# Optimization experiments

Measured on AMD Instinct MI355X. Metric: run time of the kernel, lower is better.

## Reference

```python
import jax, jax.numpy as jnp
import numpy as np

L, B, T, E, NH, HD, HID, V = 8, 2, 2048, 1024, 16, 64, 2816, 32000


def _rmsnorm(x, w, eps=1e-6):
    return w * (x * jax.lax.rsqrt(jnp.mean(x * x, axis=-1, keepdims=True) + eps))


def _rope(x, cos, sin):
    # x: [B,H,T,D]; cos/sin: [1,1,T,D/2]
    x1, x2 = jnp.split(x, 2, axis=-1)
    return jnp.concatenate([x1 * cos - x2 * sin, x1 * sin + x2 * cos], axis=-1)


def setup_inputs() -> dict:
    key = jax.random.key(0)
    ks = jax.random.split(key, 7)
    s = 0.02
    return {
        "idx": jax.random.randint(ks[0], (B, T), 0, V),
        "tok_emb": jax.random.normal(ks[1], (V, E), dtype=jnp.float32) * s,
        "qkv_w": jax.random.normal(ks[2], (L, 3 * E, E), dtype=jnp.float32) * s,
        "proj_w": jax.random.normal(ks[3], (L, E, E), dtype=jnp.float32) * s,
        "w1": jax.random.normal(ks[4], (L, HID, E), dtype=jnp.float32) * s,
        "w2": jax.random.normal(ks[5], (L, HID, E), dtype=jnp.float32) * s,
        "w3": jax.random.normal(ks[6], (L, E, HID), dtype=jnp.float32) * s,
        "norm1_w": jnp.ones((L, E), dtype=jnp.float32),
        "norm2_w": jnp.ones((L, E), dtype=jnp.float32),
        "norm_f_w": jnp.ones((E,), dtype=jnp.float32),
    }


def reference(idx, tok_emb, qkv_w, proj_w, w1, w2, w3, norm1_w, norm2_w, norm_f_w):
    x = tok_emb[idx]  # [B,T,E]
    # RoPE cache (start_pos=0, no kv cache -> prefill path)
    half = HD // 2
    inv_freq = 1.0 / (10000.0 ** (jnp.arange(half, dtype=jnp.float32) / half))
    pos = jnp.arange(T, dtype=jnp.float32)
    freqs = pos[:, None] * inv_freq[None, :]  # [T, D/2]
    cos = jnp.cos(freqs)[None, None]
    sin = jnp.sin(freqs)[None, None]
    causal = jnp.tril(jnp.ones((T, T), dtype=bool))
    scale = 1.0 / np.sqrt(HD).astype(np.float32)

    for l in range(L):
        # attention block
        h = _rmsnorm(x, norm1_w[l])
        qkv = h @ qkv_w[l].T  # [B,T,3E]
        q, k, v = jnp.split(qkv, 3, axis=-1)
        q = q.reshape(B, T, NH, HD).transpose(0, 2, 1, 3)
        k = k.reshape(B, T, NH, HD).transpose(0, 2, 1, 3)
        v = v.reshape(B, T, NH, HD).transpose(0, 2, 1, 3)
        q = _rope(q, cos, sin)
        k = _rope(k, cos, sin)
        att = jnp.einsum('bhqd,bhkd->bhqk', q, k) * scale
        att = jnp.where(causal, att, -jnp.inf)
        att = jax.nn.softmax(att, axis=-1)
        o = jnp.einsum('bhqk,bhkd->bhqd', att, v)
        o = o.transpose(0, 2, 1, 3).reshape(B, T, E)
        x = x + o @ proj_w[l].T
        # SwiGLU MLP
        h = _rmsnorm(x, norm2_w[l])
        x = x + (jax.nn.silu(h @ w1[l].T) * (h @ w2[l].T)) @ w3[l].T

    x = _rmsnorm(x, norm_f_w)
    logits = x @ tok_emb.T  # tied lm_head
    return logits
```

## Files before the change

### kernel.cpp

```cpp
#include <hip/hip_runtime.h>

#define GLOBAL_AS __attribute__((address_space(1)))
#define LDS_AS __attribute__((address_space(3)))

typedef unsigned short u16;
typedef unsigned int u32;
typedef __attribute__((ext_vector_type(4))) float f32x4;
typedef __attribute__((ext_vector_type(8))) short bf16x8;

#define TT 2048
#define EE 1024
#define NHH 16
#define HDD 64
#define HIDD 2816
#define VV 32000
#define MM 4096

__device__ __forceinline__ u16 f2bf(float f) {
  u32 u = __builtin_bit_cast(u32, f);
  u += 0x7fffu + ((u >> 16) & 1u);
  return (u16)(u >> 16);
}
__device__ __forceinline__ float bf2f(u16 v) {
  return __builtin_bit_cast(float, (u32)v << 16);
}


__global__ __launch_bounds__(256) void castbf_k(const float* __restrict__ in,
                                                u16* __restrict__ o, long n4) {
  const long i = (long)blockIdx.x * 256 + threadIdx.x;
  if (i >= n4) return;
  const float4 v = ((const float4*)in)[i];
  ((uint2*)o)[i] = make_uint2((u32)f2bf(v.x) | ((u32)f2bf(v.y) << 16),
                              (u32)f2bf(v.z) | ((u32)f2bf(v.w) << 16));
}

__global__ void ropetab_k(float* __restrict__ cosT, float* __restrict__ sinT) {
  const int t = blockIdx.x, j = threadIdx.x;
  const float inv = powf(10000.0f, -(float)j * (1.0f / 32.0f));
  const float f = (float)t * inv;
  cosT[t * 32 + j] = cosf(f);
  sinT[t * 32 + j] = sinf(f);
}

__global__ __launch_bounds__(256) void embed_k(const int* __restrict__ idx,
                                               const float* __restrict__ temb,
                                               float* __restrict__ x) {
  const int row = blockIdx.x;
  const int id = idx[row];
  ((float4*)(x + (size_t)row * EE))[threadIdx.x] =
      ((const float4*)(temb + (size_t)id * EE))[threadIdx.x];
}

__global__ __launch_bounds__(256) void rmsnorm_k(const float* __restrict__ x,
                                                 const float* __restrict__ w,
                                                 u16* __restrict__ o) {
  __shared__ float red[4];
  const int row = blockIdx.x, tid = threadIdx.x;
  const float4 v = ((const float4*)(x + (size_t)row * EE))[tid];
  float ss = v.x * v.x + v.y * v.y + v.z * v.z + v.w * v.w;
#pragma unroll
  for (int off = 32; off; off >>= 1) ss += __shfl_xor(ss, off, 64);
  if ((tid & 63) == 0) red[tid >> 6] = ss;
  __syncthreads();
  const float inv = rsqrtf((red[0] + red[1] + red[2] + red[3]) * (1.0f / 1024.0f) + 1e-6f);
  const float4 wv = ((const float4*)w)[tid];
  const u32 lo = (u32)f2bf(v.x * inv * wv.x) | ((u32)f2bf(v.y * inv * wv.y) << 16);
  const u32 hi = (u32)f2bf(v.z * inv * wv.z) | ((u32)f2bf(v.w * inv * wv.w) << 16);
  ((uint2*)(o + (size_t)row * EE))[tid] = make_uint2(lo, hi);
}

template <int OUTBF>
__global__ __launch_bounds__(512, 2) void gemm256p(const u16* __restrict__ A,
                                                   const u16* __restrict__ Bw,
                                                   float* __restrict__ C,
                                                   u16* __restrict__ C16,
                                                   const u16* __restrict__ G,
                                                   int N, int K) {
  __shared__ u16 lds[2 * 32768];
  const int t = threadIdx.x;
  const int lane = t & 63;
  const int wid = t >> 6;
  const int wr = wid >> 2;
  const int wc = wid & 3;
  const int l15 = lane & 15, lg = lane >> 4;
  const int bid = blockIdx.x;
  const int row0 = (bid & 15) << 8;
  const int col0 = (bid >> 4) << 8;
  const int NT = K >> 6;

  const int sr = t >> 3;
  const int su8 = (((t & 7) ^ (sr & 7)) << 3);
  const int t8 = t << 3;
  const u16* aG[4];
#pragma unroll
  for (int ga = 0; ga < 4; ++ga)
    aG[ga] = A + (size_t)(row0 + ga * 64 + sr) * K + su8;
  const u16* bG[4];
#pragma unroll
  for (int gb = 0; gb < 4; ++gb) {
    const int q = (gb * 2 + (sr >> 5)) & 3;
    const int nh = gb >> 1;
    bG[gb] = Bw + (size_t)(col0 + q * 64 + nh * 32 + (sr & 31)) * K + su8;
  }

  const int u0 = ((lg ^ (l15 & 7)) << 3);
  const int u1 = (((4 | lg) ^ (l15 & 7)) << 3);
  const int arow = (wr * 128 + l15) << 6;
  const int brow = 16384 + ((wc * 32 + l15) << 6);

  f32x4 acc[8][4] = {};

#define STA(nb, ga, k0n)                                                              \
  __builtin_amdgcn_global_load_lds((const GLOBAL_AS void*)(aG[ga] + (k0n)),           \
                                   (LDS_AS void*)((nb) + (ga)*4096 + t8), 16, 0, 0)
#define STB(nb, gb, k0n)                                                              \
  __builtin_amdgcn_global_load_lds((const GLOBAL_AS void*)(bG[gb] + (k0n)),           \
                                   (LDS_AS void*)((nb) + 16384 + (gb)*4096 + t8), 16, 0, 0)

  {
    u16* nb = lds;
    STA(nb, 0, 0); STA(nb, 2, 0);
    STB(nb, 0, 0); STB(nb, 1, 0);
    STB(nb, 2, 0); STB(nb, 3, 0);
    STA(nb, 1, 0); STA(nb, 3, 0);
  }

  bf16x8 af[4][2], bl[2][2], bh[2][2];

  for (int kt = 0; kt < NT; ++kt) {
    const bool st = (kt + 1 < NT);
    const int k0n = (kt + 1) << 6;
    const u16* cb = lds + (kt & 1) * 32768;
    u16* nb = lds + ((kt + 1) & 1) * 32768;

    asm volatile("s_waitcnt vmcnt(4)" ::: "memory");
    __builtin_amdgcn_s_barrier();
#pragma unroll
    for (int mi = 0; mi < 4; ++mi) {
      af[mi][0] = *(const bf16x8*)&cb[arow + mi * 1024 + u0];
      af[mi][1] = *(const bf16x8*)&cb[arow + mi * 1024 + u1];
    }
#pragma unroll
    for (int ni = 0; ni < 2; ++ni) {
      bl[ni][0] = *(const bf16x8*)&cb[brow + ni * 1024 + u0];
      bl[ni][1] = *(const bf16x8*)&cb[brow + ni * 1024 + u1];
    }
    if (st) { STA(nb, 0, k0n); STA(nb, 2, k0n); }
    __builtin_amdgcn_s_setprio(1);
#pragma unroll
    for (int mi = 0; mi < 4; ++mi)
#pragma unroll
      for (int ni = 0; ni < 2; ++ni) {
        acc[mi][ni] = __builtin_amdgcn_mfma_f32_16x16x32_bf16(af[mi][0], bl[ni][0], acc[mi][ni], 0, 0, 0);
        acc[mi][ni] = __builtin_amdgcn_mfma_f32_16x16x32_bf16(af[mi][1], bl[ni][1], acc[mi][ni], 0, 0, 0);
      }
    __builtin_amdgcn_s_setprio(0);

    if (st) { asm volatile("s_waitcnt vmcnt(4)" ::: "memory"); }
    else    { asm volatile("s_waitcnt vmcnt(2)" ::: "memory"); }
    __builtin_amdgcn_s_barrier();
#pragma unroll
    for (int ni = 0; ni < 2; ++ni) {
      bh[ni][0] = *(const bf16x8*)&cb[brow + 8192 + ni * 1024 + u0];
      bh[ni][1] = *(const bf16x8*)&cb[brow + 8192 + ni * 1024 + u1];
    }
    if (st) { STB(nb, 0, k0n); STB(nb, 1, k0n); }
    __builtin_amdgcn_s_setprio(1);
#pragma unroll
    for (int mi = 0; mi < 4; ++mi)
#pragma unroll
      for (int ni = 0; ni < 2; ++ni) {
        acc[mi][2 + ni] = __builtin_amdgcn_mfma_f32_16x16x32_bf16(af[mi][0], bh[ni][0], acc[mi][2 + ni], 0, 0, 0);
        acc[mi][2 + ni] = __builtin_amdgcn_mfma_f32_16x16x32_bf16(af[mi][1], bh[ni][1], acc[mi][2 + ni], 0, 0, 0);
      }
    __builtin_amdgcn_s_setprio(0);

    if (st) { asm volatile("s_waitcnt vmcnt(4)" ::: "memory"); }
    else    { asm volatile("s_waitcnt vmcnt(0)" ::: "memory"); }
    __builtin_amdgcn_s_barrier();
#pragma unroll
    for (int mi = 0; mi < 4; ++mi) {
      af[mi][0] = *(const bf16x8*)&cb[arow + (4 + mi) * 1024 + u0];
      af[mi][1] = *(const bf16x8*)&cb[arow + (4 + mi) * 1024 + u1];
    }
    if (st) { STB(nb, 2, k0n); STB(nb, 3, k0n); }
    __builtin_amdgcn_s_setprio(1);
#pragma unroll
    for (int mi = 0; mi < 4; ++mi)
#pragma unroll
      for (int ni = 0; ni < 2; ++ni) {
        acc[4 + mi][2 + ni] = __builtin_amdgcn_mfma_f32_16x16x32_bf16(af[mi][0], bh[ni][0], acc[4 + mi][2 + ni], 0, 0, 0);
        acc[4 + mi][2 + ni] = __builtin_amdgcn_mfma_f32_16x16x32_bf16(af[mi][1], bh[ni][1], acc[4 + mi][2 + ni], 0, 0, 0);
      }
    __builtin_amdgcn_s_setprio(0);

    if (st) { STA(nb, 1, k0n); STA(nb, 3, k0n); }
    __builtin_amdgcn_s_setprio(1);
#pragma unroll
    for (int mi = 0; mi < 4; ++mi)
#pragma unroll
      for (int ni = 0; ni < 2; ++ni) {
        acc[4 + mi][ni] = __builtin_amdgcn_mfma_f32_16x16x32_bf16(af[mi][0], bl[ni][0], acc[4 + mi][ni], 0, 0, 0);
        acc[4 + mi][ni] = __builtin_amdgcn_mfma_f32_16x16x32_bf16(af[mi][1], bl[ni][1], acc[4 + mi][ni], 0, 0, 0);
      }
    __builtin_amdgcn_s_setprio(0);
  }
#undef STA
#undef STB

#pragma unroll
  for (int m = 0; m < 8; ++m) {
    const int row = row0 + wr * 128 + m * 16 + lg * 4;
#pragma unroll
    for (int n = 0; n < 4; ++n) {
      const int col = col0 + wc * 64 + n * 16 + l15;
#pragma unroll
      for (int r = 0; r < 4; ++r) {
        const size_t o = (size_t)(row + r) * N + col;
        if (OUTBF == 0) {
          C[o] = acc[m][n][r];
        } else if (OUTBF == 1) {
          C16[o] = f2bf(acc[m][n][r]);
        } else {
          const float g = bf2f(G[o]);
          C16[o] = f2bf(g / (1.0f + __expf(-g)) * acc[m][n][r]);
        }
      }
    }
  }
}

template <int OUTBF>
__global__ __launch_bounds__(512, 2) void gemm128n(const u16* __restrict__ A,
                                                   const u16* __restrict__ Bw,
                                                   float* __restrict__ C,
                                                   const float* __restrict__ R,
                                                   u16* __restrict__ C16,
                                                   const u16* __restrict__ G,
                                                   const float* __restrict__ cosT,
                                                   const float* __restrict__ sinT,
                                                   u16* __restrict__ Qb,
                                                   u16* __restrict__ Kb,
                                                   u16* __restrict__ Vtb,
                                                   int N, int K) {
  __shared__ u16 lds[4 * 8192];
  const int t = threadIdx.x;
  const int lane = t & 63;
  const int wid = t >> 6;
  const int wr = wid & 3;
  const int wc = wid >> 2;
  const int l15 = lane & 15, lg = lane >> 4;
  const int bid = blockIdx.x;
  const int row0 = (bid & 31) << 7;
  const int col0 = (bid >> 5) << 7;
  const int NT = K >> 5;

  const int rA = t >> 2;
  const int usw = (((t & 3) ^ ((t >> 3) & 3)) << 3);
  const u16* sA = A + (size_t)(row0 + rA) * K + usw;
  const u16* sB = Bw + (size_t)(col0 + rA) * K + usw;
  const int dst = t << 3;

  const int e8 = ((lg ^ ((l15 >> 1) & 3)) << 3);
  const int aoff = (wr * 32 + l15) * 32 + e8;
  const int boff = 4096 + (wc * 64 + l15) * 32 + e8;

  f32x4 acc[2][4] = {};

  auto stage = [&](int kt) {
    u16* base = &lds[(kt & 3) * 8192];
    const size_t ko = (size_t)kt * 32;
    __builtin_amdgcn_global_load_lds((const GLOBAL_AS void*)(sA + ko),
                                     (LDS_AS void*)(base + dst), 16, 0, 0);
    __builtin_amdgcn_global_load_lds((const GLOBAL_AS void*)(sB + ko),
                                     (LDS_AS void*)(base + 4096 + dst), 16, 0, 0);
  };

  stage(0);
  stage(1);
  stage(2);

  for (int kt = 0; kt < NT; ++kt) {
    const int rem = NT - 1 - kt;
    if (rem >= 2) {
      asm volatile("s_waitcnt vmcnt(4)" ::: "memory");
    } else if (rem == 1) {
      asm volatile("s_waitcnt vmcnt(2)" ::: "memory");
    } else {
      asm volatile("s_waitcnt vmcnt(0)" ::: "memory");
    }
    __builtin_amdgcn_s_barrier();
    if (kt + 3 < NT) stage(kt + 3);
    const u16* base = &lds[(kt & 3) * 8192];
    bf16x8 af[2], bfv[4];
#pragma unroll
    for (int m = 0; m < 2; ++m) af[m] = *(const bf16x8*)&base[aoff + m * 512];
#pragma unroll
    for (int n = 0; n < 4; ++n) bfv[n] = *(const bf16x8*)&base[boff + n * 512];
    __builtin_amdgcn_s_setprio(1);
#pragma unroll
    for (int m = 0; m < 2; ++m)
#pragma unroll
      for (int n = 0; n < 4; ++n)
        acc[m][n] = __builtin_amdgcn_mfma_f32_16x16x32_bf16(af[m], bfv[n], acc[m][n], 0, 0, 0);
    __builtin_amdgcn_s_setprio(0);
  }

  if (OUTBF == 3) {
    const int reg = col0 >> 10;
    const int fb = col0 & 1023;
#pragma unroll
    for (int m = 0; m < 2; ++m) {
      const int row = row0 + wr * 32 + m * 16 + lg * 4;
      const int b = row >> 11, tbase = row & 2047;
      if (reg < 2) {
        u16* dstp = (reg == 0) ? Qb : Kb;
        const float qs = (reg == 0) ? 0.125f : 1.0f;
#pragma unroll
        for (int n = 0; n < 2; ++n) {
          const int f = fb + wc * 64 + n * 16 + l15;
          const int h = f >> 6, j = f & 63;
#pragma unroll
          for (int r = 0; r < 4; ++r) {
            const int tt = tbase + r;
            const float c = cosT[tt * 32 + j], s = sinT[tt * 32 + j];
            const float x1 = acc[m][n][r], x2 = acc[m][n | 2][r];
            const size_t ro = ((size_t)(b * NHH + h) * TT + tt) * HDD + j;
            dstp[ro] = f2bf((x1 * c - x2 * s) * qs);
            dstp[ro + 32] = f2bf((x1 * s + x2 * c) * qs);
          }
        }
      } else {
#pragma unroll
        for (int n = 0; n < 4; ++n) {
          const int f = fb + wc * 64 + n * 16 + l15;
          const int h = f >> 6, j = f & 63;
          ushort4 pk;
          pk.x = f2bf(acc[m][n][0]);
          pk.y = f2bf(acc[m][n][1]);
          pk.z = f2bf(acc[m][n][2]);
          pk.w = f2bf(acc[m][n][3]);
          *(ushort4*)&Vtb[((size_t)(b * NHH + h) * HDD + j) * TT + tbase] = pk;
        }
      }
    }
    return;
  }

#pragma unroll
  for (int m = 0; m < 2; ++m) {
    const int row = row0 + wr * 32 + m * 16 + lg * 4;
#pragma unroll
    for (int n = 0; n < 4; ++n) {
      const int col = col0 + wc * 64 + n * 16 + l15;
#pragma unroll
      for (int r = 0; r < 4; ++r) {
        const size_t o = (size_t)(row + r) * N + col;
        if (OUTBF == 0) {
          C[o] = acc[m][n][r] + R[o];
        } else if (OUTBF == 1) {
          C16[o] = f2bf(acc[m][n][r]);
        } else {
          const float g = bf2f(G[o]);
          C16[o] = f2bf(g / (1.0f + __expf(-g)) * acc[m][n][r]);
        }
      }
    }
  }
}

__global__ __launch_bounds__(256) void attn_k(const u16* __restrict__ Q,
                                              const u16* __restrict__ Kc,
                                              const u16* __restrict__ Vt,
                                              u16* __restrict__ O) {
  __shared__ u16 P_lds[4][32][72];
  const int bid = blockIdx.x;
  const int bh = bid & 31;
  const int jj = bid >> 5;
  const int qi = (bid < 256) ? jj : 23 - jj;
  const int q0 = qi << 7;
  const int lane = threadIdx.x & 63;
  const int w = threadIdx.x >> 6;
  const int l15 = lane & 15, lg = lane >> 4;
  const int qbase = q0 + w * 32;

  bf16x8 qf[2][2];
#pragma unroll
  for (int am = 0; am < 2; ++am)
#pragma unroll
    for (int ks = 0; ks < 2; ++ks)
      qf[am][ks] = *(const bf16x8*)&Q[((size_t)bh * TT + qbase + am * 16 + l15) * HDD + ks * 32 + lg * 8];

  bf16x8 ones;
#pragma unroll
  for (int i = 0; i < 8; ++i) ones[i] = (short)0x3F80;

  f32x4 oacc[2][4] = {};
  f32x4 lacc[2] = {};

  const int ntile = (q0 + 128) >> 6;
  for (int kt = 0; kt < ntile; ++kt) {
    const int k0 = kt << 6;
    f32x4 s[2][4];
    bf16x8 kf0[4], kf1[4];
#pragma unroll
    for (int an = 0; an < 4; ++an) {
      kf0[an] = *(const bf16x8*)&Kc[((size_t)bh * TT + k0 + an * 16 + l15) * HDD + lg * 8];
      kf1[an] = *(const bf16x8*)&Kc[((size_t)bh * TT + k0 + an * 16 + l15) * HDD + 32 + lg * 8];
    }
    __builtin_amdgcn_s_setprio(1);
#pragma unroll
    for (int an = 0; an < 4; ++an) {
#pragma unroll
      for (int am = 0; am < 2; ++am) {
        f32x4 z = {0.0f, 0.0f, 0.0f, 0.0f};
        z = __builtin_amdgcn_mfma_f32_16x16x32_bf16(qf[am][0], kf0[an], z, 0, 0, 0);
        s[am][an] = __builtin_amdgcn_mfma_f32_16x16x32_bf16(qf[am][1], kf1[an], z, 0, 0, 0);
      }
    }
    __builtin_amdgcn_s_setprio(0);
    const bool diag = (k0 + 64) > q0;
#pragma unroll
    for (int am = 0; am < 2; ++am)
#pragma unroll
      for (int an = 0; an < 4; ++an)
#pragma unroll
        for (int r = 0; r < 4; ++r) {
          float v = s[am][an][r];
          if (diag) {
            const int qrow = qbase + am * 16 + lg * 4 + r;
            const int kcol = k0 + an * 16 + l15;
            if (kcol > qrow) v = -1e30f;
          }
          s[am][an][r] = __expf(v);
        }
#pragma unroll
    for (int am = 0; am < 2; ++am)
#pragma unroll
      for (int an = 0; an < 4; ++an)
#pragma unroll
        for (int r = 0; r < 4; ++r)
          P_lds[w][am * 16 + lg * 4 + r][an * 16 + l15] = f2bf(s[am][an][r]);
#pragma unroll
    for (int ks = 0; ks < 2; ++ks) {
      bf16x8 pf[2];
#pragma unroll
      for (int am = 0; am < 2; ++am)
        pf[am] = *(const bf16x8*)&P_lds[w][am * 16 + l15][ks * 32 + lg * 8];
      __builtin_amdgcn_s_setprio(1);
#pragma unroll
      for (int dn = 0; dn < 4; ++dn) {
        const bf16x8 vf = *(const bf16x8*)&Vt[((size_t)bh * HDD + dn * 16 + l15) * TT + k0 + ks * 32 + lg * 8];
#pragma unroll
        for (int am = 0; am < 2; ++am)
          oacc[am][dn] = __builtin_amdgcn_mfma_f32_16x16x32_bf16(pf[am], vf, oacc[am][dn], 0, 0, 0);
      }
#pragma unroll
      for (int am = 0; am < 2; ++am)
        lacc[am] = __builtin_amdgcn_mfma_f32_16x16x32_bf16(pf[am], ones, lacc[am], 0, 0, 0);
      __builtin_amdgcn_s_setprio(0);
    }
  }
  const int b = bh >> 4, h = bh & 15;
#pragma unroll
  for (int am = 0; am < 2; ++am)
#pragma unroll
    for (int r = 0; r < 4; ++r) {
      const float il = 1.0f / lacc[am][r];
      const int qrow = qbase + am * 16 + lg * 4 + r;
#pragma unroll
      for (int dn = 0; dn < 4; ++dn)
        O[((size_t)b * TT + qrow) * EE + h * 64 + dn * 16 + l15] = f2bf(oacc[am][dn][r] * il);
    }
}


extern "C" void kernel_launch(void* const* d_in, const int* in_sizes, int n_in,
                              void* d_out, int out_size, void* d_ws, size_t ws_size,
                              hipStream_t stream) {
  const int* idx = (const int*)d_in[0];
  const float* tok_emb = (const float*)d_in[1];
  const float* qkv_w = (const float*)d_in[2];
  const float* proj_w = (const float*)d_in[3];
  const float* w1 = (const float*)d_in[4];
  const float* w2 = (const float*)d_in[5];
  const float* w3 = (const float*)d_in[6];
  const float* norm1_w = (const float*)d_in[7];
  const float* norm2_w = (const float*)d_in[8];
  const float* norm_f_w = (const float*)d_in[9];
  float* out = (float*)d_out;

  char* ws = (char*)d_ws;
  size_t off = 0;
  auto alloc = [&](size_t bytes) -> void* {
    off = (off + 255) & ~(size_t)255;
    void* p = ws + off;
    off += bytes;
    return p;
  };

  const size_t N_TEMB = (size_t)VV * EE;
  const size_t N_QKVW = (size_t)8 * 3 * EE * EE;
  const size_t N_PROJW = (size_t)8 * EE * EE;
  const size_t N_W1 = (size_t)8 * HIDD * EE;
  const size_t N_W3 = (size_t)8 * EE * HIDD;

  u16* tembbf = (u16*)alloc(N_TEMB * 2);
  u16* qkvwbf = (u16*)alloc(N_QKVW * 2);
  u16* projwbf = (u16*)alloc(N_PROJW * 2);
  u16* w1bf = (u16*)alloc(N_W1 * 2);
  u16* w2bf = (u16*)alloc(N_W1 * 2);
  u16* w3bf = (u16*)alloc(N_W3 * 2);
  float* x = (float*)alloc((size_t)MM * EE * 4);
  u16* h1 = (u16*)alloc((size_t)MM * EE * 2);
  u16* hg = (u16*)alloc((size_t)MM * HIDD * 2);
  u16* qb = (u16*)alloc((size_t)2 * NHH * TT * HDD * 2);
  u16* kb = (u16*)alloc((size_t)2 * NHH * TT * HDD * 2);
  u16* vtb = (u16*)alloc((size_t)2 * NHH * TT * HDD * 2);
  u16* attno = (u16*)alloc((size_t)MM * EE * 2);
  float* cosT = (float*)alloc((size_t)TT * 32 * 4);
  float* sinT = (float*)alloc((size_t)TT * 32 * 4);

  u16* g16 = (u16*)(out + 16777216);

  auto cast = [&](const float* src, u16* dst, size_t n) {
    const long n4 = (long)(n / 4);
    castbf_k<<<(int)((n4 + 255) / 256), 256, 0, stream>>>(src, dst, n4);
  };
  cast(tok_emb, tembbf, N_TEMB);
  cast(qkv_w, qkvwbf, N_QKVW);
  cast(proj_w, projwbf, N_PROJW);
  cast(w1, w1bf, N_W1);
  cast(w2, w2bf, N_W1);
  cast(w3, w3bf, N_W3);

  ropetab_k<<<TT, 32, 0, stream>>>(cosT, sinT);
  embed_k<<<MM, 256, 0, stream>>>(idx, tok_emb, x);

  for (int l = 0; l < 8; ++l) {
    rmsnorm_k<<<MM, 256, 0, stream>>>(x, norm1_w + l * EE, h1);
    gemm128n<3><<<dim3(24 * 32), 512, 0, stream>>>(h1, qkvwbf + (size_t)l * 3 * EE * EE,
                                                   nullptr, nullptr, nullptr, nullptr,
                                                   cosT, sinT, qb, kb, vtb, 3 * EE, EE);
    attn_k<<<dim3(512), 256, 0, stream>>>(qb, kb, vtb, attno);
    gemm128n<0><<<dim3(8 * 32), 512, 0, stream>>>(attno, projwbf + (size_t)l * EE * EE,
                                                  x, x, nullptr, nullptr,
                                                  nullptr, nullptr, nullptr, nullptr, nullptr,
                                                  EE, EE);
    rmsnorm_k<<<MM, 256, 0, stream>>>(x, norm2_w + l * EE, h1);
    gemm128n<1><<<dim3(22 * 32), 512, 0, stream>>>(h1, w1bf + (size_t)l * HIDD * EE,
                                                   nullptr, nullptr, g16, nullptr,
                                                   nullptr, nullptr, nullptr, nullptr, nullptr,
                                                   HIDD, EE);
    gemm128n<2><<<dim3(22 * 32), 512, 0, stream>>>(h1, w2bf + (size_t)l * HIDD * EE,
                                                   nullptr, nullptr, hg, g16,
                                                   nullptr, nullptr, nullptr, nullptr, nullptr,
                                                   HIDD, EE);
    gemm128n<0><<<dim3(8 * 32), 512, 0, stream>>>(hg, w3bf + (size_t)l * EE * HIDD,
                                                  x, x, nullptr, nullptr,
                                                  nullptr, nullptr, nullptr, nullptr, nullptr,
                                                  EE, HIDD);
  }
  rmsnorm_k<<<MM, 256, 0, stream>>>(x, norm_f_w, h1);
  gemm256p<0><<<dim3(125 * 16), 512, 0, stream>>>(h1, tembbf, out, nullptr, nullptr,
                                                  VV, EE);
}
```

Baseline: 2.568 ms.

## Fuse gate and up MLP GEMMs into one dual-weight kernel; use exp2 in attention

Replaces the two separate SwiGLU GEMMs, where the first wrote bf16 gate values and the second reread them, with one kernel that computes the gate and up tiles together. It shares the A tile in LDS and applies SiLU times up in the epilogue. This removes the intermediate gate round-trip through global memory and one launch per layer. Attention folds log2(e) into the Q scale so it can use raw v_exp_f32, and packs P to bf16 with v_cvt_pk_bf16_f32. The fused kernel uses 128x64 output tiles with a triple-buffered pipeline, which changes occupancy and tiling behaviour.

Measured after the change: 2.420 ms, median of 3. 5.8% less time.

```diff
diff --git a/kernel.cpp b/kernel.cpp
--- a/kernel.cpp
+++ b/kernel.cpp
@@ -236,8 +236,6 @@
                                                    const u16* __restrict__ Bw,
                                                    float* __restrict__ C,
                                                    const float* __restrict__ R,
-                                                   u16* __restrict__ C16,
-                                                   const u16* __restrict__ G,
                                                    const float* __restrict__ cosT,
                                                    const float* __restrict__ sinT,
                                                    u16* __restrict__ Qb,
@@ -316,7 +314,7 @@
       const int b = row >> 11, tbase = row & 2047;
       if (reg < 2) {
         u16* dstp = (reg == 0) ? Qb : Kb;
-        const float qs = (reg == 0) ? 0.125f : 1.0f;
+        const float qs = (reg == 0) ? 0.18033688011112042f : 1.0f;
 #pragma unroll
         for (int n = 0; n < 2; ++n) {
           const int f = fb + wc * 64 + n * 16 + l15;
@@ -357,14 +355,101 @@
 #pragma unroll
       for (int r = 0; r < 4; ++r) {
         const size_t o = (size_t)(row + r) * N + col;
-        if (OUTBF == 0) {
-          C[o] = acc[m][n][r] + R[o];
-        } else if (OUTBF == 1) {
-          C16[o] = f2bf(acc[m][n][r]);
-        } else {
-          const float g = bf2f(G[o]);
-          C16[o] = f2bf(g / (1.0f + __expf(-g)) * acc[m][n][r]);
-        }
+        C[o] = acc[m][n][r] + R[o];
+      }
+    }
+  }
+}
+
+__global__ __launch_bounds__(512, 2) void gemm128d(const u16* __restrict__ A,
+                                                   const u16* __restrict__ Bg,
+                                                   const u16* __restrict__ Bu,
+                                                   u16* __restrict__ C16,
+                                                   int N, int K) {
+  __shared__ u16 lds[3 * 8192];
+  const int t = threadIdx.x;
+  const int lane = t & 63;
+  const int wid = t >> 6;
+  const int wr = wid & 3;
+  const int wc = wid >> 2;
+  const int l15 = lane & 15, lg = lane >> 4;
+  const int bid = blockIdx.x;
+  const int row0 = (bid & 31) << 7;
+  const int col0 = (bid >> 5) << 6;
+  const int NT = K >> 5;
+
+  const int rA = t >> 2;
+  const int usw = (((t & 3) ^ ((t >> 3) & 3)) << 3);
+  const u16* sA = A + (size_t)(row0 + rA) * K + usw;
+  const int tb = t & 255;
+  const int rB = tb >> 2;
+  const int uswB = (((tb & 3) ^ ((tb >> 3) & 3)) << 3);
+  const u16* sB = ((wid < 4) ? Bg : Bu) + (size_t)(col0 + rB) * K + uswB;
+  const int dstA = t << 3;
+  const int dstB = 4096 + ((wid < 4) ? 0 : 2048) + (tb << 3);
+
+  const int e8 = ((lg ^ ((l15 >> 1) & 3)) << 3);
+  const int aoff = (wr * 32 + l15) * 32 + e8;
+  const int goff = 4096 + (wc * 32 + l15) * 32 + e8;
+  const int uoff = 6144 + (wc * 32 + l15) * 32 + e8;
+
+  f32x4 ag[2][2] = {}, au[2][2] = {};
+
+  auto stage = [&](int kt, int buf) {
+    u16* b = &lds[buf * 8192];
+    const size_t ko = (size_t)kt * 32;
+    __builtin_amdgcn_global_load_lds((const GLOBAL_AS void*)(sA + ko),
+                                     (LDS_AS void*)(b + dstA), 16, 0, 0);
+    __builtin_amdgcn_global_load_lds((const GLOBAL_AS void*)(sB + ko),
+                                     (LDS_AS void*)(b + dstB), 16, 0, 0);
+  };
+
+  stage(0, 0);
+  stage(1, 1);
+
+  int cbuf = 0;
+  for (int kt = 0; kt < NT; ++kt) {
+    if (kt + 1 < NT) {
+      asm volatile("s_waitcnt vmcnt(2)" ::: "memory");
+    } else {
+      asm volatile("s_waitcnt vmcnt(0)" ::: "memory");
+    }
+    __builtin_amdgcn_s_barrier();
+    const int nbuf = (cbuf == 2) ? 0 : cbuf + 1;
+    const int sbuf = (nbuf == 2) ? 0 : nbuf + 1;
+    if (kt + 2 < NT) stage(kt + 2, sbuf);
+    const u16* cb = &lds[cbuf * 8192];
+    bf16x8 af[2], bgv[2], buv[2];
+#pragma unroll
+    for (int m = 0; m < 2; ++m) af[m] = *(const bf16x8*)&cb[aoff + m * 512];
+#pragma unroll
+    for (int n = 0; n < 2; ++n) {
+      bgv[n] = *(const bf16x8*)&cb[goff + n * 512];
+      buv[n] = *(const bf16x8*)&cb[uoff + n * 512];
+    }
+    __builtin_amdgcn_s_setprio(1);
+#pragma unroll
+    for (int m = 0; m < 2; ++m)
+#pragma unroll
+      for (int n = 0; n < 2; ++n) {
+        ag[m][n] = __builtin_amdgcn_mfma_f32_16x16x32_bf16(af[m], bgv[n], ag[m][n], 0, 0, 0);
+        au[m][n] = __builtin_amdgcn_mfma_f32_16x16x32_bf16(af[m], buv[n], au[m][n], 0, 0, 0);
+      }
+    __builtin_amdgcn_s_setprio(0);
+    cbuf = nbuf;
+  }
+
+#pragma unroll
+  for (int m = 0; m < 2; ++m) {
+    const int row = row0 + wr * 32 + m * 16 + lg * 4;
+#pragma unroll
+    for (int n = 0; n < 2; ++n) {
+      const int col = col0 + wc * 32 + n * 16 + l15;
+#pragma unroll
+      for (int r = 0; r < 4; ++r) {
+        const float g = ag[m][n][r];
+        const float u = au[m][n][r];
+        C16[(size_t)(row + r) * N + col] = f2bf(g / (1.0f + __expf(-g)) * u);
       }
     }
   }
@@ -433,15 +518,23 @@
             const int kcol = k0 + an * 16 + l15;
             if (kcol > qrow) v = -1e30f;
           }
-          s[am][an][r] = __expf(v);
+          float p;
+          asm("v_exp_f32 %0, %1" : "=v"(p) : "v"(v));
+          s[am][an][r] = p;
         }
 #pragma unroll
     for (int am = 0; am < 2; ++am)
 #pragma unroll
       for (int an = 0; an < 4; ++an)
 #pragma unroll
-        for (int r = 0; r < 4; ++r)
-          P_lds[w][am * 16 + lg * 4 + r][an * 16 + l15] = f2bf(s[am][an][r]);
+        for (int rp = 0; rp < 2; ++rp) {
+          u32 pk;
+          asm("v_cvt_pk_bf16_f32 %0, %1, %2"
+              : "=v"(pk) : "v"(s[am][an][2 * rp]), "v"(s[am][an][2 * rp + 1]));
+          const int rowb = am * 16 + lg * 4 + 2 * rp;
+          P_lds[w][rowb][an * 16 + l15] = (u16)pk;
+          P_lds[w][rowb + 1][an * 16 + l15] = (u16)(pk >> 16);
+        }
 #pragma unroll
     for (int ks = 0; ks < 2; ++ks) {
       bf16x8 pf[2];
@@ -522,8 +615,6 @@
   float* cosT = (float*)alloc((size_t)TT * 32 * 4);
   float* sinT = (float*)alloc((size_t)TT * 32 * 4);
 
-  u16* g16 = (u16*)(out + 16777216);
-
   auto cast = [&](const float* src, u16* dst, size_t n) {
     const long n4 = (long)(n / 4);
     castbf_k<<<(int)((n4 + 255) / 256), 256, 0, stream>>>(src, dst, n4);
@@ -541,24 +632,19 @@
   for (int l = 0; l < 8; ++l) {
     rmsnorm_k<<<MM, 256, 0, stream>>>(x, norm1_w + l * EE, h1);
     gemm128n<3><<<dim3(24 * 32), 512, 0, stream>>>(h1, qkvwbf + (size_t)l * 3 * EE * EE,
-                                                   nullptr, nullptr, nullptr, nullptr,
+                                                   nullptr, nullptr,
                                                    cosT, sinT, qb, kb, vtb, 3 * EE, EE);
     attn_k<<<dim3(512), 256, 0, stream>>>(qb, kb, vtb, attno);
     gemm128n<0><<<dim3(8 * 32), 512, 0, stream>>>(attno, projwbf + (size_t)l * EE * EE,
-                                                  x, x, nullptr, nullptr,
+                                                  x, x,
                                                   nullptr, nullptr, nullptr, nullptr, nullptr,
                                                   EE, EE);
     rmsnorm_k<<<MM, 256, 0, stream>>>(x, norm2_w + l * EE, h1);
-    gemm128n<1><<<dim3(22 * 32), 512, 0, stream>>>(h1, w1bf + (size_t)l * HIDD * EE,
-                                                   nullptr, nullptr, g16, nullptr,
-                                                   nullptr, nullptr, nullptr, nullptr, nullptr,
-                                                   HIDD, EE);
-    gemm128n<2><<<dim3(22 * 32), 512, 0, stream>>>(h1, w2bf + (size_t)l * HIDD * EE,
-                                                   nullptr, nullptr, hg, g16,
-                                                   nullptr, nullptr, nullptr, nullptr, nullptr,
-                                                   HIDD, EE);
+    gemm128d<<<dim3(44 * 32), 512, 0, stream>>>(h1, w1bf + (size_t)l * HIDD * EE,
+                                                w2bf + (size_t)l * HIDD * EE,
+                                                hg, HIDD, EE);
     gemm128n<0><<<dim3(8 * 32), 512, 0, stream>>>(hg, w3bf + (size_t)l * EE * HIDD,
-                                                  x, x, nullptr, nullptr,
+                                                  x, x,
                                                   nullptr, nullptr, nullptr, nullptr, nullptr,
                                                   EE, HIDD);
   }
```
